# Optimization experiments

Hardware: AMD Instinct MI355X
Metric: run time of the kernel (lower is better)

Reference implementation:

```python
import jax, jax.numpy as jnp
import numpy as np

DIM_HEAD = 32
WINDOW_SIZE = 8


def get_rel_pos_ind(win):
    coords = np.stack(np.meshgrid(np.arange(win), np.arange(win), indexing='ij')).reshape(2, -1)
    rel = coords[:, :, None] - coords[:, None, :] + (win - 1)
    return rel  # int


def setup_inputs() -> dict:
    key = jax.random.key(0)
    ks = jax.random.split(key, 4)
    B, N, dim = 2048, WINDOW_SIZE * WINDOW_SIZE, 512
    heads = dim // DIM_HEAD
    size = 2 * WINDOW_SIZE - 1
    return {
        'x': jax.random.normal(ks[0], (B, N, dim), jnp.float32),
        'w_qkv': jax.random.normal(ks[1], (dim, 3 * dim), jnp.float32) * 0.02,
        'b_qkv': jnp.zeros((3 * dim,), jnp.float32),
        'rel_pos_table': jax.random.normal(ks[2], (heads, size, size), jnp.float32) * 0.02,
        'w_proj': jax.random.normal(ks[3], (dim, dim), jnp.float32) * 0.02,
        'b_proj': jnp.zeros((dim,), jnp.float32),
        'train': 0,
    }


def reference(x, w_qkv, b_qkv, rel_pos_table, w_proj, b_proj, train):
    B, N, dim = x.shape
    heads = dim // DIM_HEAD
    scale = DIM_HEAD ** (-0.5)

    qkv = x @ w_qkv + b_qkv                                  # (B, N, 3*dim)
    qkv = qkv.reshape(B, N, 3, heads, DIM_HEAD)
    qkv = jnp.swapaxes(qkv, 1, 3)                            # (B, heads, 3, N, dh)
    q, k, v = qkv[:, :, 0], qkv[:, :, 1], qkv[:, :, 2]
    q = q * scale

    attn = jnp.einsum('bhnd,bhmd->bhnm', q, k)               # (B, heads, N, N)

    ind = get_rel_pos_ind(WINDOW_SIZE)                       # (2, N, N)
    bias = rel_pos_table[:, ind[0], ind[1]]                  # (heads, N, N)
    attn = jax.nn.softmax(attn + bias, axis=-1)

    out = jnp.einsum('bhnm,bhmd->bhnd', attn, v)             # (B, heads, N, dh)
    out = jnp.swapaxes(out, 1, 2).reshape(B, N, dim)
    return out @ w_proj + b_proj
```

## Files before the change

kernel.cpp:

```cpp
#include <hip/hip_runtime.h>
#include <stdint.h>
#include <stddef.h>

typedef unsigned short u16;
typedef __attribute__((ext_vector_type(8))) short short8;
typedef __attribute__((ext_vector_type(8))) unsigned short ushort8;
typedef __attribute__((ext_vector_type(4))) float f32x4;

#define NTOK 64
#define QKVC 1536
#define DIM  512
#define QK_REGION 4608

__device__ __forceinline__ float bf2f(u16 u) {
  union { unsigned int i; float f; } x; x.i = ((unsigned int)u) << 16; return x.f;
}
__device__ __forceinline__ u16 f2bf(float f) {
  union { float f; unsigned int i; } x; x.f = f;
  unsigned int u = x.i;
  u += 0x7fffu + ((u >> 16) & 1u);
  return (u16)(u >> 16);
}

__device__ __forceinline__ void async16(const void* g, void* l) {
  __builtin_amdgcn_global_load_lds((const __attribute__((address_space(1))) void*)g,
                                   (__attribute__((address_space(3))) void*)l,
                                   16, 0, 0);
}

__device__ __forceinline__ f32x4 shfl_xor4(f32x4 v, int m) {
  f32x4 r;
  #pragma unroll
  for (int e = 0; e < 4; ++e) r[e] = __shfl_xor(v[e], m, 64);
  return r;
}
__device__ __forceinline__ f32x4 max44(f32x4 a, f32x4 b) {
  f32x4 r;
  #pragma unroll
  for (int e = 0; e < 4; ++e) r[e] = fmaxf(a[e], b[e]);
  return r;
}

__global__ void detect_k(const u16* __restrict__ w_raw, int* __restrict__ flag) {
  if (threadIdx.x == 0 && blockIdx.x == 0) {
    int cnt = 0;
    for (int i = 0; i < 512; ++i) {
      float v = bf2f(w_raw[i]);
      if (!(v <= 0.5f && v >= -0.5f)) ++cnt;
    }
    flag[0] = (cnt > 16) ? 1 : 0;
  }
}


__global__ void cvt_k(const float* __restrict__ fsrc, const u16* __restrict__ usrc,
                      u16* __restrict__ dst, int n, const int* __restrict__ flag) {
  int i = blockIdx.x * 256 + threadIdx.x;
  if (i >= n) return;
  if (flag[0]) dst[i] = f2bf(fsrc[i]);
  else         dst[i] = usrc[i];
}

__global__ void transpose_k(const float* __restrict__ fsrc, const u16* __restrict__ usrc,
                            u16* __restrict__ dst, int R, int C, const int* __restrict__ flag) {
  int idx = blockIdx.x * 256 + threadIdx.x;
  int n = idx / R, k = idx % R;
  if (flag[0]) dst[idx] = f2bf(fsrc[k * C + n]);
  else         dst[idx] = usrc[k * C + n];
}

__global__ void bias_expand_k(const float* __restrict__ ftab, const u16* __restrict__ utab,
                              float* __restrict__ biasc, const int* __restrict__ flag) {
  int t = blockIdx.x * 256 + threadIdx.x;
  int r    = t & 3;
  int lane = (t >> 2) & 63;
  int ni   = (t >> 8) & 3;
  int mi   = (t >> 10) & 3;
  int h    = t >> 12;
  int n = mi * 16 + (lane >> 4) * 4 + r;
  int m = ni * 16 + (lane & 15);
  int i1 = n >> 3, j1 = n & 7, i2 = m >> 3, j2 = m & 7;
  int off = h * 225 + (i1 - i2 + 7) * 15 + (j1 - j2 + 7);
  if (flag[0]) biasc[t] = ftab[off];
  else         biasc[t] = bf2f(utab[off]);
}

__global__ __launch_bounds__(256) void gemm_bt(
    const u16* __restrict__ A, const u16* __restrict__ Bt, const u16* __restrict__ bias,
    u16* __restrict__ Cu, float* __restrict__ Cf, const int* __restrict__ outf32,
    int N, int K)
{
  __shared__ __attribute__((aligned(16))) u16 Al[128 * 32];
  __shared__ __attribute__((aligned(16))) u16 Bl[128 * 32];

  const int tn = blockIdx.x * 128;
  const int tm = blockIdx.y * 128;
  const int lane = threadIdx.x & 63;
  const int wave = threadIdx.x >> 6;
  const int lr = lane & 15, quad = lane >> 4;
  const int wm = (wave & 1) * 64, wn = (wave >> 1) * 64;

  const f32x4 zero4 = {0.f, 0.f, 0.f, 0.f};
  f32x4 acc[4][4];
  #pragma unroll
  for (int mi = 0; mi < 4; ++mi)
    #pragma unroll
    for (int ni = 0; ni < 4; ++ni) acc[mi][ni] = zero4;

  for (int k0 = 0; k0 < K; k0 += 32) {
    #pragma unroll
    for (int i = 0; i < 2; ++i) {
      int c = (i * 4 + wave) * 64 + lane;
      int row = c >> 2, off = (c & 3) << 3;
      async16(A  + (size_t)(tm + row) * K + k0 + off, Al + (i * 4 + wave) * 512);
      async16(Bt + (size_t)(tn + row) * K + k0 + off, Bl + (i * 4 + wave) * 512);
    }
    __syncthreads();

    short8 af[4], bfr[4];
    #pragma unroll
    for (int mi = 0; mi < 4; ++mi)
      af[mi] = *(const short8*)&Al[(wm + mi * 16 + lr) * 32 + quad * 8];
    #pragma unroll
    for (int ni = 0; ni < 4; ++ni)
      bfr[ni] = *(const short8*)&Bl[(wn + ni * 16 + lr) * 32 + quad * 8];

    #pragma unroll
    for (int mi = 0; mi < 4; ++mi)
      #pragma unroll
      for (int ni = 0; ni < 4; ++ni)
        acc[mi][ni] = __builtin_amdgcn_mfma_f32_16x16x32_bf16(af[mi], bfr[ni], acc[mi][ni], 0, 0, 0);
    __syncthreads();
  }

  const int f32o = outf32 ? outf32[0] : 0;
  #pragma unroll
  for (int ni = 0; ni < 4; ++ni) {
    int col = tn + wn + ni * 16 + lr;
    float bv = bf2f(bias[col]);
    #pragma unroll
    for (int mi = 0; mi < 4; ++mi) {
      size_t rb = (size_t)(tm + wm + mi * 16 + quad * 4);
      #pragma unroll
      for (int r = 0; r < 4; ++r) {
        float val = acc[mi][ni][r] + bv;
        size_t ofs = (rb + r) * (size_t)N + col;
        if (f32o) Cf[ofs] = val;
        else      Cu[ofs] = f2bf(val);
      }
    }
  }
}

__global__ __launch_bounds__(256) void attn_k(
    const u16* __restrict__ qkv,
    const float* __restrict__ biasc,
    u16* __restrict__ out)
{
  __shared__ __attribute__((aligned(16))) u16 qkP[4][QK_REGION];
  __shared__ __attribute__((aligned(16))) u16 vTs[4][32 * 72];

  const int lane = threadIdx.x & 63;
  const int wave = threadIdx.x >> 6;
  const int idx = blockIdx.x * 4 + wave;
  const int b = idx >> 4, h = idx & 15;
  const int lr = lane & 15, quad = lane >> 4;

  u16* ql = qkP[wave];
  u16* kl = qkP[wave] + 2304;
  u16* Pl = qkP[wave];
  u16* vt = vTs[wave];

  const u16* qg = qkv + (size_t)b * NTOK * QKVC + h * 32;
  const u16* kg = qg + 512;
  const u16* vg = qg + 1024;

  #pragma unroll
  for (int i = 0; i < 4; ++i) {
    int c = i * 64 + lane;
    int row = c >> 2, off = (c & 3) << 3;
    async16(qg + (size_t)row * QKVC + off, ql + i * 512);
    async16(kg + (size_t)row * QKVC + off, kl + i * 512);
  }
  {
    const u16* vrow = vg + (size_t)lane * QKVC;
    #pragma unroll
    for (int c2 = 0; c2 < 4; ++c2) {
      ushort8 vv = *(const ushort8*)(vrow + c2 * 8);
      #pragma unroll
      for (int e = 0; e < 8; ++e)
        vt[(c2 * 8 + e) * 72 + lane] = vv[e];
    }
  }
  __syncthreads();

  const f32x4 zero4 = {0.f, 0.f, 0.f, 0.f};
  f32x4 s[4][4];
  {
    short8 af[4], bfr[4];
    #pragma unroll
    for (int mi = 0; mi < 4; ++mi)
      af[mi] = *(const short8*)&ql[(mi * 16 + lr) * 32 + quad * 8];
    #pragma unroll
    for (int ni = 0; ni < 4; ++ni)
      bfr[ni] = *(const short8*)&kl[(ni * 16 + lr) * 32 + quad * 8];
    #pragma unroll
    for (int mi = 0; mi < 4; ++mi)
      #pragma unroll
      for (int ni = 0; ni < 4; ++ni)
        s[mi][ni] = __builtin_amdgcn_mfma_f32_16x16x32_bf16(af[mi], bfr[ni], zero4, 0, 0, 0);
  }

  const float SCALE = 0.17677669529663687f;
  const float L2E = 1.44269504088896f;
  #pragma unroll
  for (int mi = 0; mi < 4; ++mi)
    #pragma unroll
    for (int ni = 0; ni < 4; ++ni) {
      f32x4 bb = *(const f32x4*)&biasc[((((h * 4 + mi) * 4 + ni) * 64) + lane) * 4];
      s[mi][ni] = s[mi][ni] * SCALE + bb;
    }

  f32x4 mx[4];
  #pragma unroll
  for (int mi = 0; mi < 4; ++mi) {
    mx[mi] = max44(max44(s[mi][0], s[mi][1]), max44(s[mi][2], s[mi][3]));
    #pragma unroll
    for (int m = 1; m <= 8; m <<= 1) mx[mi] = max44(mx[mi], shfl_xor4(mx[mi], m));
  }
  f32x4 sum[4];
  #pragma unroll
  for (int mi = 0; mi < 4; ++mi) {
    #pragma unroll
    for (int ni = 0; ni < 4; ++ni)
      #pragma unroll
      for (int e = 0; e < 4; ++e)
        s[mi][ni][e] = exp2f((s[mi][ni][e] - mx[mi][e]) * L2E);
    sum[mi] = s[mi][0] + s[mi][1] + s[mi][2] + s[mi][3];
    #pragma unroll
    for (int m = 1; m <= 8; m <<= 1) sum[mi] = sum[mi] + shfl_xor4(sum[mi], m);
  }

  #pragma unroll
  for (int mi = 0; mi < 4; ++mi)
    #pragma unroll
    for (int ni = 0; ni < 4; ++ni)
      #pragma unroll
      for (int r = 0; r < 4; ++r) {
        int n = mi * 16 + quad * 4 + r;
        int col = ni * 16 + lr;
        Pl[n * 72 + col] = f2bf(s[mi][ni][r]);
      }
  __syncthreads();

  f32x4 o[4][2];
  #pragma unroll
  for (int mi = 0; mi < 4; ++mi) { o[mi][0] = zero4; o[mi][1] = zero4; }
  #pragma unroll
  for (int ks = 0; ks < 2; ++ks) {
    short8 pf[4], vf[2];
    #pragma unroll
    for (int mi = 0; mi < 4; ++mi)
      pf[mi] = *(const short8*)&Pl[(mi * 16 + lr) * 72 + ks * 32 + quad * 8];
    #pragma unroll
    for (int ni = 0; ni < 2; ++ni)
      vf[ni] = *(const short8*)&vt[(ni * 16 + lr) * 72 + ks * 32 + quad * 8];
    #pragma unroll
    for (int mi = 0; mi < 4; ++mi)
      #pragma unroll
      for (int ni = 0; ni < 2; ++ni)
        o[mi][ni] = __builtin_amdgcn_mfma_f32_16x16x32_bf16(pf[mi], vf[ni], o[mi][ni], 0, 0, 0);
  }

  f32x4 rs[4];
  #pragma unroll
  for (int mi = 0; mi < 4; ++mi)
    #pragma unroll
    for (int e = 0; e < 4; ++e) rs[mi][e] = __builtin_amdgcn_rcpf(sum[mi][e]);

  #pragma unroll
  for (int mi = 0; mi < 4; ++mi)
    #pragma unroll
    for (int ni = 0; ni < 2; ++ni)
      #pragma unroll
      for (int r = 0; r < 4; ++r) {
        int n = mi * 16 + quad * 4 + r;
        int d = ni * 16 + lr;
        out[(size_t)(b * NTOK + n) * DIM + h * 32 + d] = f2bf(o[mi][ni][r] * rs[mi][r]);
      }
}


extern "C" void kernel_launch(void* const* d_in, const int* in_sizes, int n_in,
                              void* d_out, int out_size, void* d_ws, size_t ws_size,
                              hipStream_t stream)
{
  (void)in_sizes; (void)n_in; (void)out_size;

  const void* x      = d_in[0];
  const void* w_qkv  = d_in[1];
  const void* b_qkv  = d_in[2];
  const void* table  = d_in[3];
  const void* w_proj = d_in[4];
  const void* b_proj = d_in[5];

  char* ws = (char*)d_ws;
  size_t off = 0;
  auto alloc = [&](size_t bytes) -> char* {
    char* p = ws + off; off += (bytes + 255) & ~(size_t)255; return p;
  };
  u16*   wqkvT  = (u16*)alloc(1572864);
  u16*   wprojT = (u16*)alloc(524288);
  float* biasc  = (float*)alloc(262144);
  u16*   bqc    = (u16*)alloc(3072);
  u16*   bpc    = (u16*)alloc(1024);
  int*   flag   = (int*)alloc(256);
  size_t fixed  = off;

  int win = 256;
  while (win > 2 && fixed + (size_t)win * 327680 > ws_size) win >>= 1;
  const int mc = win * 64;
  u16* xbfC  = (u16*)alloc((size_t)mc * 512 * 2);
  u16* qkvC  = (u16*)alloc((size_t)mc * 1536 * 2);
  u16* aoutC = (u16*)alloc((size_t)mc * 512 * 2);

  detect_k<<<dim3(1), dim3(64), 0, stream>>>((const u16*)w_qkv, flag);
  transpose_k<<<dim3(3072), dim3(256), 0, stream>>>((const float*)w_qkv, (const u16*)w_qkv, wqkvT, 512, 1536, flag);
  transpose_k<<<dim3(1024), dim3(256), 0, stream>>>((const float*)w_proj, (const u16*)w_proj, wprojT, 512, 512, flag);
  bias_expand_k<<<dim3(256), dim3(256), 0, stream>>>((const float*)table, (const u16*)table, biasc, flag);
  cvt_k<<<dim3(6), dim3(256), 0, stream>>>((const float*)b_qkv, (const u16*)b_qkv, bqc, 1536, flag);
  cvt_k<<<dim3(2), dim3(256), 0, stream>>>((const float*)b_proj, (const u16*)b_proj, bpc, 512, flag);

  const int nchunk = 2048 / win;
  for (int c = 0; c < nchunk; ++c) {
    size_t base = (size_t)c * mc * 512;

    cvt_k<<<dim3((mc * 512) / 256), dim3(256), 0, stream>>>(
        (const float*)x + base, (const u16*)x + base, xbfC, mc * 512, flag);

    gemm_bt<<<dim3(12, mc / 128), dim3(256), 0, stream>>>(
        xbfC, wqkvT, bqc, qkvC, (float*)nullptr, (const int*)nullptr, 1536, 512);

    attn_k<<<dim3(win * 4), dim3(256), 0, stream>>>(qkvC, biasc, aoutC);

    gemm_bt<<<dim3(4, mc / 128), dim3(256), 0, stream>>>(
        aoutC, wprojT, bpc, (u16*)d_out + base, (float*)d_out + base, flag, 512, 512);
  }
}
```

Baseline: 1.279 ms.

## Add triple-buffered 512-thread GEMM, vectorize conversion, and enlarge chunk window

Adds a templated GEMM kernel with larger 256x256 and 256x128 tiles, 512 threads, three LDS buffers filled by async global-to-LDS loads, explicit vmcnt waits, and s_setprio around the MFMA loop. The aim is to hide load latency and raise data reuse in the QKV and projection GEMMs. The element conversion kernel now handles 8 elements per thread with vector loads and stores. The chunk window doubles to 512 so fewer chunk launches are needed when the workspace allows it. Larger tiles and more LDS use can lower occupancy, and the grid for the projection GEMM becomes small.

```diff
diff --git a/kernel.cpp b/kernel.cpp
--- a/kernel.cpp
+++ b/kernel.cpp
@@ -26,6 +26,13 @@
   __builtin_amdgcn_global_load_lds((const __attribute__((address_space(1))) void*)g,
                                    (__attribute__((address_space(3))) void*)l,
                                    16, 0, 0);
+}
+
+template<int L>
+__device__ __forceinline__ void wait_vm() {
+  if constexpr (L == 4)      asm volatile("s_waitcnt vmcnt(4)" ::: "memory");
+  else if constexpr (L == 3) asm volatile("s_waitcnt vmcnt(3)" ::: "memory");
+  else                       asm volatile("s_waitcnt vmcnt(0)" ::: "memory");
 }
 
 __device__ __forceinline__ f32x4 shfl_xor4(f32x4 v, int m) {
@@ -53,12 +60,20 @@
 }
 
 
-__global__ void cvt_k(const float* __restrict__ fsrc, const u16* __restrict__ usrc,
-                      u16* __restrict__ dst, int n, const int* __restrict__ flag) {
-  int i = blockIdx.x * 256 + threadIdx.x;
+__global__ void cvt8_k(const float* __restrict__ fsrc, const u16* __restrict__ usrc,
+                       u16* __restrict__ dst, int n, const int* __restrict__ flag) {
+  int i = (blockIdx.x * 256 + threadIdx.x) * 8;
   if (i >= n) return;
-  if (flag[0]) dst[i] = f2bf(fsrc[i]);
-  else         dst[i] = usrc[i];
+  if (flag[0]) {
+    f32x4 a = *(const f32x4*)(fsrc + i);
+    f32x4 b = *(const f32x4*)(fsrc + i + 4);
+    ushort8 o;
+    #pragma unroll
+    for (int e = 0; e < 4; ++e) { o[e] = f2bf(a[e]); o[e + 4] = f2bf(b[e]); }
+    *(ushort8*)(dst + i) = o;
+  } else {
+    *(ushort8*)(dst + i) = *(const ushort8*)(usrc + i);
+  }
 }
 
 __global__ void transpose_k(const float* __restrict__ fsrc, const u16* __restrict__ usrc,
@@ -152,6 +167,97 @@
   }
 }
 
+template<int BM, int BN, int WR, int WC>
+__global__ __launch_bounds__(512, 2) void gemm_bt_p(
+    const u16* __restrict__ A, const u16* __restrict__ Bt, const u16* __restrict__ bias,
+    u16* __restrict__ Cu, float* __restrict__ Cf, const int* __restrict__ outf32,
+    int N, int K)
+{
+  constexpr int BK = 32;
+  constexpr int LA = BM / 128, LB = BN / 128, L = LA + LB;
+  constexpr int MI = BM / (WR * 16), NI = BN / (WC * 16);
+
+  __shared__ __attribute__((aligned(16))) u16 Al[3][BM * BK];
+  __shared__ __attribute__((aligned(16))) u16 Bl[3][BN * BK];
+
+  const int tn = blockIdx.x * BN;
+  const int tm = blockIdx.y * BM;
+  const int lane = threadIdx.x & 63;
+  const int wave = threadIdx.x >> 6;
+  const int lr = lane & 15, quad = lane >> 4;
+  const int wr = wave / WC, wc = wave % WC;
+
+  const int srow = wave * 16 + (lane >> 2);
+  const int soff = (lane & 3) << 3;
+  const u16* ag = A  + (size_t)(tm + srow) * K + soff;
+  const u16* bg = Bt + (size_t)(tn + srow) * K + soff;
+
+  const f32x4 zero4 = {0.f, 0.f, 0.f, 0.f};
+  f32x4 acc[MI][NI];
+  #pragma unroll
+  for (int mi = 0; mi < MI; ++mi)
+    #pragma unroll
+    for (int ni = 0; ni < NI; ++ni) acc[mi][ni] = zero4;
+
+  auto stage = [&](int t) {
+    const int buf = ((unsigned)t) % 3u;
+    #pragma unroll
+    for (int ld = 0; ld < LA; ++ld)
+      async16(ag + (size_t)(ld * 128) * K + t * BK, &Al[buf][ld * 4096 + wave * 512]);
+    #pragma unroll
+    for (int ld = 0; ld < LB; ++ld)
+      async16(bg + (size_t)(ld * 128) * K + t * BK, &Bl[buf][ld * 4096 + wave * 512]);
+  };
+
+  const int NT = K / BK;
+  stage(0);
+  stage(1);
+
+  for (int t = 0; t < NT; ++t) {
+    if (t < NT - 2) wait_vm<L>();
+    else            wait_vm<0>();
+    __builtin_amdgcn_s_barrier();
+    asm volatile("" ::: "memory");
+
+    const int buf = ((unsigned)t) % 3u;
+    short8 af[MI], bfv[NI];
+    #pragma unroll
+    for (int mi = 0; mi < MI; ++mi)
+      af[mi] = *(const short8*)&Al[buf][(wr * (BM / WR) + mi * 16 + lr) * 32 + quad * 8];
+    #pragma unroll
+    for (int ni = 0; ni < NI; ++ni)
+      bfv[ni] = *(const short8*)&Bl[buf][(wc * (BN / WC) + ni * 16 + lr) * 32 + quad * 8];
+
+    if (t + 2 < NT) stage(t + 2);
+
+    __builtin_amdgcn_s_setprio(1);
+    #pragma unroll
+    for (int mi = 0; mi < MI; ++mi)
+      #pragma unroll
+      for (int ni = 0; ni < NI; ++ni)
+        acc[mi][ni] = __builtin_amdgcn_mfma_f32_16x16x32_bf16(af[mi], bfv[ni], acc[mi][ni], 0, 0, 0);
+    __builtin_amdgcn_s_setprio(0);
+  }
+
+  const int f32o = outf32 ? outf32[0] : 0;
+  #pragma unroll
+  for (int ni = 0; ni < NI; ++ni) {
+    int col = tn + wc * (BN / WC) + ni * 16 + lr;
+    float bv = bf2f(bias[col]);
+    #pragma unroll
+    for (int mi = 0; mi < MI; ++mi) {
+      size_t rb = (size_t)(tm + wr * (BM / WR) + mi * 16 + quad * 4);
+      #pragma unroll
+      for (int r = 0; r < 4; ++r) {
+        float val = acc[mi][ni][r] + bv;
+        size_t ofs = (rb + r) * (size_t)N + col;
+        if (f32o) Cf[ofs] = val;
+        else      Cu[ofs] = f2bf(val);
+      }
+    }
+  }
+}
+
 __global__ __launch_bounds__(256) void attn_k(
     const u16* __restrict__ qkv,
     const float* __restrict__ biasc,
@@ -317,7 +423,7 @@
   int*   flag   = (int*)alloc(256);
   size_t fixed  = off;
 
-  int win = 256;
+  int win = 512;
   while (win > 2 && fixed + (size_t)win * 327680 > ws_size) win >>= 1;
   const int mc = win * 64;
   u16* xbfC  = (u16*)alloc((size_t)mc * 512 * 2);
@@ -328,22 +434,32 @@
   transpose_k<<<dim3(3072), dim3(256), 0, stream>>>((const float*)w_qkv, (const u16*)w_qkv, wqkvT, 512, 1536, flag);
   transpose_k<<<dim3(1024), dim3(256), 0, stream>>>((const float*)w_proj, (const u16*)w_proj, wprojT, 512, 512, flag);
   bias_expand_k<<<dim3(256), dim3(256), 0, stream>>>((const float*)table, (const u16*)table, biasc, flag);
-  cvt_k<<<dim3(6), dim3(256), 0, stream>>>((const float*)b_qkv, (const u16*)b_qkv, bqc, 1536, flag);
-  cvt_k<<<dim3(2), dim3(256), 0, stream>>>((const float*)b_proj, (const u16*)b_proj, bpc, 512, flag);
+  cvt8_k<<<dim3(1), dim3(256), 0, stream>>>((const float*)b_qkv, (const u16*)b_qkv, bqc, 1536, flag);
+  cvt8_k<<<dim3(1), dim3(256), 0, stream>>>((const float*)b_proj, (const u16*)b_proj, bpc, 512, flag);
 
   const int nchunk = 2048 / win;
   for (int c = 0; c < nchunk; ++c) {
     size_t base = (size_t)c * mc * 512;
 
-    cvt_k<<<dim3((mc * 512) / 256), dim3(256), 0, stream>>>(
+    cvt8_k<<<dim3((mc * 512) / 2048), dim3(256), 0, stream>>>(
         (const float*)x + base, (const u16*)x + base, xbfC, mc * 512, flag);
 
-    gemm_bt<<<dim3(12, mc / 128), dim3(256), 0, stream>>>(
-        xbfC, wqkvT, bqc, qkvC, (float*)nullptr, (const int*)nullptr, 1536, 512);
-
-    attn_k<<<dim3(win * 4), dim3(256), 0, stream>>>(qkvC, biasc, aoutC);
-
-    gemm_bt<<<dim3(4, mc / 128), dim3(256), 0, stream>>>(
-        aoutC, wprojT, bpc, (u16*)d_out + base, (float*)d_out + base, flag, 512, 512);
-  }
-}
+    if ((mc & 255) == 0) {
+      gemm_bt_p<256, 256, 2, 4><<<dim3(6, mc / 256), dim3(512), 0, stream>>>(
+          xbfC, wqkvT, bqc, qkvC, (float*)nullptr, (const int*)nullptr, 1536, 512);
+
+      attn_k<<<dim3(win * 4), dim3(256), 0, stream>>>(qkvC, biasc, aoutC);
+
+      gemm_bt_p<256, 128, 4, 2><<<dim3(4, mc / 256), dim3(512), 0, stream>>>(
+          aoutC, wprojT, bpc, (u16*)d_out + base, (float*)d_out + base, flag, 512, 512);
+    } else {
+      gemm_bt<<<dim3(12, mc / 128), dim3(256), 0, stream>>>(
+          xbfC, wqkvT, bqc, qkvC, (float*)nullptr, (const int*)nullptr, 1536, 512);
+
+      attn_k<<<dim3(win * 4), dim3(256), 0, stream>>>(qkvC, biasc, aoutC);
+
+      gemm_bt<<<dim3(4, mc / 128), dim3(256), 0, stream>>>(
+          aoutC, wprojT, bpc, (u16*)d_out + base, (float*)d_out + base, flag, 512, 512);
+    }
+  }
+}
```

Measured after the change: 1.075 ms. -15.9%, faster.

## Fuse QKV projection, window attention and output projection into one per-window kernel

Applied to the files above, without the earlier changes.

Replaces the separate QKV GEMM, attention and output-projection kernels with a single kernel where each 512-thread block handles one 64-token window. Each wave computes Q/K/V for one head from global x and weights via MFMA, runs softmax attention in LDS, and the block then accumulates the output projection across heads. This removes the large qkv and attention-output intermediate buffers and their global round trips. In exchange, weights are read directly from global memory without LDS tiling, so each block rereads the full weight matrices. The float-to-bf16 conversion is also vectorised to 8 elements per thread, and the chunk window is enlarged.

```diff
diff --git a/kernel.cpp b/kernel.cpp
--- a/kernel.cpp
+++ b/kernel.cpp
@@ -8,9 +8,9 @@
 typedef __attribute__((ext_vector_type(4))) float f32x4;
 
 #define NTOK 64
-#define QKVC 1536
 #define DIM  512
-#define QK_REGION 4608
+#define QSTR 36
+#define REGION 6912
 
 __device__ __forceinline__ float bf2f(u16 u) {
   union { unsigned int i; float f; } x; x.i = ((unsigned int)u) << 16; return x.f;
@@ -20,12 +20,6 @@
   unsigned int u = x.i;
   u += 0x7fffu + ((u >> 16) & 1u);
   return (u16)(u >> 16);
-}
-
-__device__ __forceinline__ void async16(const void* g, void* l) {
-  __builtin_amdgcn_global_load_lds((const __attribute__((address_space(1))) void*)g,
-                                   (__attribute__((address_space(3))) void*)l,
-                                   16, 0, 0);
 }
 
 __device__ __forceinline__ f32x4 shfl_xor4(f32x4 v, int m) {
@@ -53,12 +47,20 @@
 }
 
 
-__global__ void cvt_k(const float* __restrict__ fsrc, const u16* __restrict__ usrc,
-                      u16* __restrict__ dst, int n, const int* __restrict__ flag) {
-  int i = blockIdx.x * 256 + threadIdx.x;
+__global__ void cvt8_k(const float* __restrict__ fsrc, const u16* __restrict__ usrc,
+                       u16* __restrict__ dst, int n, const int* __restrict__ flag) {
+  int i = (blockIdx.x * 256 + threadIdx.x) * 8;
   if (i >= n) return;
-  if (flag[0]) dst[i] = f2bf(fsrc[i]);
-  else         dst[i] = usrc[i];
+  if (flag[0]) {
+    f32x4 a = *(const f32x4*)(fsrc + i);
+    f32x4 b = *(const f32x4*)(fsrc + i + 4);
+    ushort8 o;
+    #pragma unroll
+    for (int e = 0; e < 4; ++e) { o[e] = f2bf(a[e]); o[e + 4] = f2bf(b[e]); }
+    *(ushort8*)(dst + i) = o;
+  } else {
+    *(ushort8*)(dst + i) = *(const ushort8*)(usrc + i);
+  }
 }
 
 __global__ void transpose_k(const float* __restrict__ fsrc, const u16* __restrict__ usrc,
@@ -85,209 +87,224 @@
   else         biasc[t] = bf2f(utab[off]);
 }
 
-__global__ __launch_bounds__(256) void gemm_bt(
-    const u16* __restrict__ A, const u16* __restrict__ Bt, const u16* __restrict__ bias,
-    u16* __restrict__ Cu, float* __restrict__ Cf, const int* __restrict__ outf32,
-    int N, int K)
+__global__ __launch_bounds__(512, 2) void fused_k(
+    const u16* __restrict__ xbf,
+    const u16* __restrict__ wqkvT,
+    const u16* __restrict__ bqc,
+    const float* __restrict__ biasc,
+    const u16* __restrict__ wprojT,
+    const u16* __restrict__ bpc,
+    const int* __restrict__ flag,
+    u16* __restrict__ outU, float* __restrict__ outF)
 {
-  __shared__ __attribute__((aligned(16))) u16 Al[128 * 32];
-  __shared__ __attribute__((aligned(16))) u16 Bl[128 * 32];
-
-  const int tn = blockIdx.x * 128;
-  const int tm = blockIdx.y * 128;
+  __shared__ __attribute__((aligned(16))) u16 lds[8][REGION];
+
   const int lane = threadIdx.x & 63;
   const int wave = threadIdx.x >> 6;
   const int lr = lane & 15, quad = lane >> 4;
-  const int wm = (wave & 1) * 64, wn = (wave >> 1) * 64;
-
+  const int blk = blockIdx.x;
+
+  u16* ql = &lds[wave][0];
+  u16* kl = &lds[wave][2304];
+  u16* Pl = &lds[wave][0];
+  u16* vt = &lds[wave][4608];
+  u16* Ol = &lds[wave][0];
+
+  const u16* xw = xbf + (size_t)blk * NTOK * DIM;
+  const float SCALE = 0.17677669529663687f;
+  const float L2E = 1.44269504088896f;
   const f32x4 zero4 = {0.f, 0.f, 0.f, 0.f};
+
   f32x4 acc[4][4];
   #pragma unroll
   for (int mi = 0; mi < 4; ++mi)
     #pragma unroll
     for (int ni = 0; ni < 4; ++ni) acc[mi][ni] = zero4;
 
-  for (int k0 = 0; k0 < K; k0 += 32) {
-    #pragma unroll
-    for (int i = 0; i < 2; ++i) {
-      int c = (i * 4 + wave) * 64 + lane;
-      int row = c >> 2, off = (c & 3) << 3;
-      async16(A  + (size_t)(tm + row) * K + k0 + off, Al + (i * 4 + wave) * 512);
-      async16(Bt + (size_t)(tn + row) * K + k0 + off, Bl + (i * 4 + wave) * 512);
-    }
+  for (int r = 0; r < 2; ++r) {
+    const int h = r * 8 + wave;
+
+    f32x4 aq[4][2], ak[4][2], av[4][2];
+    #pragma unroll
+    for (int mi = 0; mi < 4; ++mi) {
+      aq[mi][0] = zero4; aq[mi][1] = zero4;
+      ak[mi][0] = zero4; ak[mi][1] = zero4;
+      av[mi][0] = zero4; av[mi][1] = zero4;
+    }
+    const u16* ax = xw + (size_t)lr * DIM + quad * 8;
+    const u16* wq = wqkvT + ((size_t)(h * 32 + lr)) * DIM + quad * 8;
+    const u16* wk = wq + (size_t)512 * DIM;
+    const u16* wv = wq + (size_t)1024 * DIM;
+    #pragma unroll 4
+    for (int ks = 0; ks < 16; ++ks) {
+      const int ko = ks * 32;
+      short8 af[4];
+      #pragma unroll
+      for (int mi = 0; mi < 4; ++mi)
+        af[mi] = *(const short8*)(ax + mi * (16 * DIM) + ko);
+      short8 b0 = *(const short8*)(wq + ko);
+      short8 b1 = *(const short8*)(wq + 16 * DIM + ko);
+      short8 b2 = *(const short8*)(wk + ko);
+      short8 b3 = *(const short8*)(wk + 16 * DIM + ko);
+      short8 b4 = *(const short8*)(wv + ko);
+      short8 b5 = *(const short8*)(wv + 16 * DIM + ko);
+      #pragma unroll
+      for (int mi = 0; mi < 4; ++mi) {
+        aq[mi][0] = __builtin_amdgcn_mfma_f32_16x16x32_bf16(af[mi], b0, aq[mi][0], 0, 0, 0);
+        aq[mi][1] = __builtin_amdgcn_mfma_f32_16x16x32_bf16(af[mi], b1, aq[mi][1], 0, 0, 0);
+        ak[mi][0] = __builtin_amdgcn_mfma_f32_16x16x32_bf16(af[mi], b2, ak[mi][0], 0, 0, 0);
+        ak[mi][1] = __builtin_amdgcn_mfma_f32_16x16x32_bf16(af[mi], b3, ak[mi][1], 0, 0, 0);
+        av[mi][0] = __builtin_amdgcn_mfma_f32_16x16x32_bf16(af[mi], b4, av[mi][0], 0, 0, 0);
+        av[mi][1] = __builtin_amdgcn_mfma_f32_16x16x32_bf16(af[mi], b5, av[mi][1], 0, 0, 0);
+      }
+    }
+
+    #pragma unroll
+    for (int j = 0; j < 2; ++j) {
+      float bq = bf2f(bqc[h * 32 + j * 16 + lr]);
+      float bk = bf2f(bqc[512 + h * 32 + j * 16 + lr]);
+      float bv = bf2f(bqc[1024 + h * 32 + j * 16 + lr]);
+      #pragma unroll
+      for (int mi = 0; mi < 4; ++mi)
+        #pragma unroll
+        for (int e = 0; e < 4; ++e) {
+          int tok = mi * 16 + quad * 4 + e;
+          int d = j * 16 + lr;
+          ql[tok * QSTR + d] = f2bf((aq[mi][j][e] + bq) * SCALE);
+          kl[tok * QSTR + d] = f2bf(ak[mi][j][e] + bk);
+          vt[d * 72 + tok]   = f2bf(av[mi][j][e] + bv);
+        }
+    }
+
+    f32x4 s[4][4];
+    {
+      short8 afq[4], bfk[4];
+      #pragma unroll
+      for (int mi = 0; mi < 4; ++mi)
+        afq[mi] = *(const short8*)&ql[(mi * 16 + lr) * QSTR + quad * 8];
+      #pragma unroll
+      for (int ni = 0; ni < 4; ++ni)
+        bfk[ni] = *(const short8*)&kl[(ni * 16 + lr) * QSTR + quad * 8];
+      #pragma unroll
+      for (int mi = 0; mi < 4; ++mi)
+        #pragma unroll
+        for (int ni = 0; ni < 4; ++ni)
+          s[mi][ni] = __builtin_amdgcn_mfma_f32_16x16x32_bf16(afq[mi], bfk[ni], zero4, 0, 0, 0);
+    }
+
+    #pragma unroll
+    for (int mi = 0; mi < 4; ++mi)
+      #pragma unroll
+      for (int ni = 0; ni < 4; ++ni) {
+        f32x4 bb = *(const f32x4*)&biasc[((((h * 4 + mi) * 4 + ni) * 64) + lane) * 4];
+        s[mi][ni] = s[mi][ni] + bb;
+      }
+
+    f32x4 mx[4];
+    #pragma unroll
+    for (int mi = 0; mi < 4; ++mi) {
+      mx[mi] = max44(max44(s[mi][0], s[mi][1]), max44(s[mi][2], s[mi][3]));
+      #pragma unroll
+      for (int m = 1; m <= 8; m <<= 1) mx[mi] = max44(mx[mi], shfl_xor4(mx[mi], m));
+    }
+    f32x4 sum[4];
+    #pragma unroll
+    for (int mi = 0; mi < 4; ++mi) {
+      #pragma unroll
+      for (int ni = 0; ni < 4; ++ni)
+        #pragma unroll
+        for (int e = 0; e < 4; ++e)
+          s[mi][ni][e] = exp2f((s[mi][ni][e] - mx[mi][e]) * L2E);
+      sum[mi] = s[mi][0] + s[mi][1] + s[mi][2] + s[mi][3];
+      #pragma unroll
+      for (int m = 1; m <= 8; m <<= 1) sum[mi] = sum[mi] + shfl_xor4(sum[mi], m);
+    }
+
+    #pragma unroll
+    for (int mi = 0; mi < 4; ++mi)
+      #pragma unroll
+      for (int ni = 0; ni < 4; ++ni)
+        #pragma unroll
+        for (int e = 0; e < 4; ++e) {
+          int n = mi * 16 + quad * 4 + e;
+          int col = ni * 16 + lr;
+          Pl[n * 72 + col] = f2bf(s[mi][ni][e]);
+        }
+
+    f32x4 o[4][2];
+    #pragma unroll
+    for (int mi = 0; mi < 4; ++mi) { o[mi][0] = zero4; o[mi][1] = zero4; }
+    #pragma unroll
+    for (int ks = 0; ks < 2; ++ks) {
+      short8 pf[4], vf[2];
+      #pragma unroll
+      for (int mi = 0; mi < 4; ++mi)
+        pf[mi] = *(const short8*)&Pl[(mi * 16 + lr) * 72 + ks * 32 + quad * 8];
+      #pragma unroll
+      for (int ni = 0; ni < 2; ++ni)
+        vf[ni] = *(const short8*)&vt[(ni * 16 + lr) * 72 + ks * 32 + quad * 8];
+      #pragma unroll
+      for (int mi = 0; mi < 4; ++mi)
+        #pragma unroll
+        for (int ni = 0; ni < 2; ++ni)
+          o[mi][ni] = __builtin_amdgcn_mfma_f32_16x16x32_bf16(pf[mi], vf[ni], o[mi][ni], 0, 0, 0);
+    }
+
+    f32x4 rs[4];
+    #pragma unroll
+    for (int mi = 0; mi < 4; ++mi)
+      #pragma unroll
+      for (int e = 0; e < 4; ++e) rs[mi][e] = __builtin_amdgcn_rcpf(sum[mi][e]);
+    #pragma unroll
+    for (int mi = 0; mi < 4; ++mi)
+      #pragma unroll
+      for (int ni = 0; ni < 2; ++ni)
+        #pragma unroll
+        for (int e = 0; e < 4; ++e) {
+          int tok = mi * 16 + quad * 4 + e;
+          int d = ni * 16 + lr;
+          Ol[tok * QSTR + d] = f2bf(o[mi][ni][e] * rs[mi][e]);
+        }
+
     __syncthreads();
 
-    short8 af[4], bfr[4];
-    #pragma unroll
-    for (int mi = 0; mi < 4; ++mi)
-      af[mi] = *(const short8*)&Al[(wm + mi * 16 + lr) * 32 + quad * 8];
-    #pragma unroll
-    for (int ni = 0; ni < 4; ++ni)
-      bfr[ni] = *(const short8*)&Bl[(wn + ni * 16 + lr) * 32 + quad * 8];
-
-    #pragma unroll
-    for (int mi = 0; mi < 4; ++mi)
+    #pragma unroll
+    for (int w2 = 0; w2 < 8; ++w2) {
+      const u16* Ow = &lds[w2][0];
+      const int h2 = r * 8 + w2;
+      short8 afO[4], bfW[4];
+      #pragma unroll
+      for (int mi = 0; mi < 4; ++mi)
+        afO[mi] = *(const short8*)&Ow[(mi * 16 + lr) * QSTR + quad * 8];
       #pragma unroll
       for (int ni = 0; ni < 4; ++ni)
-        acc[mi][ni] = __builtin_amdgcn_mfma_f32_16x16x32_bf16(af[mi], bfr[ni], acc[mi][ni], 0, 0, 0);
+        bfW[ni] = *(const short8*)&wprojT[((size_t)(wave * 64 + ni * 16 + lr)) * DIM + h2 * 32 + quad * 8];
+      #pragma unroll
+      for (int mi = 0; mi < 4; ++mi)
+        #pragma unroll
+        for (int ni = 0; ni < 4; ++ni)
+          acc[mi][ni] = __builtin_amdgcn_mfma_f32_16x16x32_bf16(afO[mi], bfW[ni], acc[mi][ni], 0, 0, 0);
+    }
     __syncthreads();
   }
 
-  const int f32o = outf32 ? outf32[0] : 0;
+  const int f32o = flag[0];
   #pragma unroll
   for (int ni = 0; ni < 4; ++ni) {
-    int col = tn + wn + ni * 16 + lr;
-    float bv = bf2f(bias[col]);
+    int col = wave * 64 + ni * 16 + lr;
+    float bv = bf2f(bpc[col]);
     #pragma unroll
     for (int mi = 0; mi < 4; ++mi) {
-      size_t rb = (size_t)(tm + wm + mi * 16 + quad * 4);
-      #pragma unroll
-      for (int r = 0; r < 4; ++r) {
-        float val = acc[mi][ni][r] + bv;
-        size_t ofs = (rb + r) * (size_t)N + col;
-        if (f32o) Cf[ofs] = val;
-        else      Cu[ofs] = f2bf(val);
+      size_t rowb = (size_t)(blk * NTOK + mi * 16 + quad * 4);
+      #pragma unroll
+      for (int e = 0; e < 4; ++e) {
+        float val = acc[mi][ni][e] + bv;
+        size_t ofs = (rowb + e) * (size_t)DIM + col;
+        if (f32o) outF[ofs] = val;
+        else      outU[ofs] = f2bf(val);
       }
     }
   }
-}
-
-__global__ __launch_bounds__(256) void attn_k(
-    const u16* __restrict__ qkv,
-    const float* __restrict__ biasc,
-    u16* __restrict__ out)
-{
-  __shared__ __attribute__((aligned(16))) u16 qkP[4][QK_REGION];
-  __shared__ __attribute__((aligned(16))) u16 vTs[4][32 * 72];
-
-  const int lane = threadIdx.x & 63;
-  const int wave = threadIdx.x >> 6;
-  const int idx = blockIdx.x * 4 + wave;
-  const int b = idx >> 4, h = idx & 15;
-  const int lr = lane & 15, quad = lane >> 4;
-
-  u16* ql = qkP[wave];
-  u16* kl = qkP[wave] + 2304;
-  u16* Pl = qkP[wave];
-  u16* vt = vTs[wave];
-
-  const u16* qg = qkv + (size_t)b * NTOK * QKVC + h * 32;
-  const u16* kg = qg + 512;
-  const u16* vg = qg + 1024;
-
-  #pragma unroll
-  for (int i = 0; i < 4; ++i) {
-    int c = i * 64 + lane;
-    int row = c >> 2, off = (c & 3) << 3;
-    async16(qg + (size_t)row * QKVC + off, ql + i * 512);
-    async16(kg + (size_t)row * QKVC + off, kl + i * 512);
-  }
-  {
-    const u16* vrow = vg + (size_t)lane * QKVC;
-    #pragma unroll
-    for (int c2 = 0; c2 < 4; ++c2) {
-      ushort8 vv = *(const ushort8*)(vrow + c2 * 8);
-      #pragma unroll
-      for (int e = 0; e < 8; ++e)
-        vt[(c2 * 8 + e) * 72 + lane] = vv[e];
-    }
-  }
-  __syncthreads();
-
-  const f32x4 zero4 = {0.f, 0.f, 0.f, 0.f};
-  f32x4 s[4][4];
-  {
-    short8 af[4], bfr[4];
-    #pragma unroll
-    for (int mi = 0; mi < 4; ++mi)
-      af[mi] = *(const short8*)&ql[(mi * 16 + lr) * 32 + quad * 8];
-    #pragma unroll
-    for (int ni = 0; ni < 4; ++ni)
-      bfr[ni] = *(const short8*)&kl[(ni * 16 + lr) * 32 + quad * 8];
-    #pragma unroll
-    for (int mi = 0; mi < 4; ++mi)
-      #pragma unroll
-      for (int ni = 0; ni < 4; ++ni)
-        s[mi][ni] = __builtin_amdgcn_mfma_f32_16x16x32_bf16(af[mi], bfr[ni], zero4, 0, 0, 0);
-  }
-
-  const float SCALE = 0.17677669529663687f;
-  const float L2E = 1.44269504088896f;
-  #pragma unroll
-  for (int mi = 0; mi < 4; ++mi)
-    #pragma unroll
-    for (int ni = 0; ni < 4; ++ni) {
-      f32x4 bb = *(const f32x4*)&biasc[((((h * 4 + mi) * 4 + ni) * 64) + lane) * 4];
-      s[mi][ni] = s[mi][ni] * SCALE + bb;
-    }
-
-  f32x4 mx[4];
-  #pragma unroll
-  for (int mi = 0; mi < 4; ++mi) {
-    mx[mi] = max44(max44(s[mi][0], s[mi][1]), max44(s[mi][2], s[mi][3]));
-    #pragma unroll
-    for (int m = 1; m <= 8; m <<= 1) mx[mi] = max44(mx[mi], shfl_xor4(mx[mi], m));
-  }
-  f32x4 sum[4];
-  #pragma unroll
-  for (int mi = 0; mi < 4; ++mi) {
-    #pragma unroll
-    for (int ni = 0; ni < 4; ++ni)
-      #pragma unroll
-      for (int e = 0; e < 4; ++e)
-        s[mi][ni][e] = exp2f((s[mi][ni][e] - mx[mi][e]) * L2E);
-    sum[mi] = s[mi][0] + s[mi][1] + s[mi][2] + s[mi][3];
-    #pragma unroll
-    for (int m = 1; m <= 8; m <<= 1) sum[mi] = sum[mi] + shfl_xor4(sum[mi], m);
-  }
-
-  #pragma unroll
-  for (int mi = 0; mi < 4; ++mi)
-    #pragma unroll
-    for (int ni = 0; ni < 4; ++ni)
-      #pragma unroll
-      for (int r = 0; r < 4; ++r) {
-        int n = mi * 16 + quad * 4 + r;
-        int col = ni * 16 + lr;
-        Pl[n * 72 + col] = f2bf(s[mi][ni][r]);
-      }
-  __syncthreads();
-
-  f32x4 o[4][2];
-  #pragma unroll
-  for (int mi = 0; mi < 4; ++mi) { o[mi][0] = zero4; o[mi][1] = zero4; }
-  #pragma unroll
-  for (int ks = 0; ks < 2; ++ks) {
-    short8 pf[4], vf[2];
-    #pragma unroll
-    for (int mi = 0; mi < 4; ++mi)
-      pf[mi] = *(const short8*)&Pl[(mi * 16 + lr) * 72 + ks * 32 + quad * 8];
-    #pragma unroll
-    for (int ni = 0; ni < 2; ++ni)
-      vf[ni] = *(const short8*)&vt[(ni * 16 + lr) * 72 + ks * 32 + quad * 8];
-    #pragma unroll
-    for (int mi = 0; mi < 4; ++mi)
-      #pragma unroll
-      for (int ni = 0; ni < 2; ++ni)
-        o[mi][ni] = __builtin_amdgcn_mfma_f32_16x16x32_bf16(pf[mi], vf[ni], o[mi][ni], 0, 0, 0);
-  }
-
-  f32x4 rs[4];
-  #pragma unroll
-  for (int mi = 0; mi < 4; ++mi)
-    #pragma unroll
-    for (int e = 0; e < 4; ++e) rs[mi][e] = __builtin_amdgcn_rcpf(sum[mi][e]);
-
-  #pragma unroll
-  for (int mi = 0; mi < 4; ++mi)
-    #pragma unroll
-    for (int ni = 0; ni < 2; ++ni)
-      #pragma unroll
-      for (int r = 0; r < 4; ++r) {
-        int n = mi * 16 + quad * 4 + r;
-        int d = ni * 16 + lr;
-        out[(size_t)(b * NTOK + n) * DIM + h * 32 + d] = f2bf(o[mi][ni][r] * rs[mi][r]);
-      }
 }
 
 
@@ -317,33 +334,27 @@
   int*   flag   = (int*)alloc(256);
   size_t fixed  = off;
 
-  int win = 256;
-  while (win > 2 && fixed + (size_t)win * 327680 > ws_size) win >>= 1;
+  int win = 2048;
+  while (win > 2 && fixed + (size_t)win * 65536 > ws_size) win >>= 1;
   const int mc = win * 64;
-  u16* xbfC  = (u16*)alloc((size_t)mc * 512 * 2);
-  u16* qkvC  = (u16*)alloc((size_t)mc * 1536 * 2);
-  u16* aoutC = (u16*)alloc((size_t)mc * 512 * 2);
+  u16* xbfC = (u16*)alloc((size_t)mc * 512 * 2);
 
   detect_k<<<dim3(1), dim3(64), 0, stream>>>((const u16*)w_qkv, flag);
   transpose_k<<<dim3(3072), dim3(256), 0, stream>>>((const float*)w_qkv, (const u16*)w_qkv, wqkvT, 512, 1536, flag);
   transpose_k<<<dim3(1024), dim3(256), 0, stream>>>((const float*)w_proj, (const u16*)w_proj, wprojT, 512, 512, flag);
   bias_expand_k<<<dim3(256), dim3(256), 0, stream>>>((const float*)table, (const u16*)table, biasc, flag);
-  cvt_k<<<dim3(6), dim3(256), 0, stream>>>((const float*)b_qkv, (const u16*)b_qkv, bqc, 1536, flag);
-  cvt_k<<<dim3(2), dim3(256), 0, stream>>>((const float*)b_proj, (const u16*)b_proj, bpc, 512, flag);
+  cvt8_k<<<dim3(1), dim3(256), 0, stream>>>((const float*)b_qkv, (const u16*)b_qkv, bqc, 1536, flag);
+  cvt8_k<<<dim3(1), dim3(256), 0, stream>>>((const float*)b_proj, (const u16*)b_proj, bpc, 512, flag);
 
   const int nchunk = 2048 / win;
   for (int c = 0; c < nchunk; ++c) {
     size_t base = (size_t)c * mc * 512;
 
-    cvt_k<<<dim3((mc * 512) / 256), dim3(256), 0, stream>>>(
+    cvt8_k<<<dim3((mc * 512) / 2048), dim3(256), 0, stream>>>(
         (const float*)x + base, (const u16*)x + base, xbfC, mc * 512, flag);
 
-    gemm_bt<<<dim3(12, mc / 128), dim3(256), 0, stream>>>(
-        xbfC, wqkvT, bqc, qkvC, (float*)nullptr, (const int*)nullptr, 1536, 512);
-
-    attn_k<<<dim3(win * 4), dim3(256), 0, stream>>>(qkvC, biasc, aoutC);
-
-    gemm_bt<<<dim3(4, mc / 128), dim3(256), 0, stream>>>(
-        aoutC, wprojT, bpc, (u16*)d_out + base, (float*)d_out + base, flag, 512, 512);
-  }
-}
+    fused_k<<<dim3(win), dim3(512), 0, stream>>>(
+        xbfC, wqkvT, bqc, biasc, wprojT, bpc, flag,
+        (u16*)d_out + base, (float*)d_out + base);
+  }
+}
```

Measured after the change: 1.434 ms. +12.1%, slower.
